# Kernel optimization log

Measured on AMD Instinct MI355X. Metric: run time of the kernel, lower is better.

Reference implementation:

```python
import jax, jax.numpy as jnp
import numpy as np

# 7 axial hex directions (dy, dx) including center, matching HexConv2d.DIRS
DIRS = [(0, 0), (1, 0), (0, 1), (-1, 1), (-1, 0), (0, -1), (1, -1)]


def _shift(x, dy, dx):
    """torch.roll-style shift with zero fill at wrapped edges. x: [B,C,H,W]."""
    sx, sy = -dx, -dy
    y = jnp.roll(x, shift=(sy, sx), axis=(2, 3))
    if sy > 0:
        y = y.at[:, :, :sy, :].set(0)
    elif sy < 0:
        y = y.at[:, :, sy:, :].set(0)
    if sx > 0:
        y = y.at[:, :, :, :sx].set(0)
    elif sx < 0:
        y = y.at[:, :, :, sx:].set(0)
    return y


def _hex_mask(H, dtype):
    size = H // 2
    q = jnp.arange(-size, size + 1)
    Q, R = jnp.meshgrid(q, q, indexing='ij')
    S = -Q - R
    # |Q|<=size and |R|<=size hold by construction; only |S|<=size cuts corners
    mask = ((jnp.abs(Q) <= size) & (jnp.abs(R) <= size) & (jnp.abs(S) <= size))
    return mask.astype(dtype)[None, None]  # [1,1,H,W]


def setup_inputs() -> dict:
    key = jax.random.key(0)
    k1, k2, k3 = jax.random.split(key, 3)
    B, Cin, Cout, H = 32, 256, 256, 49
    x = jax.random.normal(k1, (B, Cin, H, H), dtype=jnp.float32)
    weight = jax.random.normal(k2, (Cout, Cin, 7), dtype=jnp.float32) * 0.02
    bias = jax.random.normal(k3, (Cout,), dtype=jnp.float32) * 0.02
    return {"x": x, "weight": weight, "bias": bias}


def reference(x, weight, bias):
    mask = _hex_mask(x.shape[2], x.dtype)          # [1,1,H,W]
    x = x * mask
    # [7,B,C,H,W]: shifted+masked neighbor maps
    nbr = jnp.stack([_shift(x, dy, dx) for (dy, dx) in DIRS], axis=0) * mask
    # fused 1x1 conv over (channel, direction): weight [O,C,7]
    y = jnp.einsum('nbchw,ocn->bohw', nbr, weight) + bias[None, :, None, None]
    return y * mask
```

## Files before the change

### kernel.cpp

```cpp
#include <hip/hip_runtime.h>


typedef __attribute__((ext_vector_type(8))) short short8;
typedef __attribute__((ext_vector_type(4))) float floatx4;

#define NPIX   2401
#define PTILE  64
#define NPT    38
#define NSEG   11
#define WINROWS (NSEG*16)
#define ZROW   176
#define PADROWS 2560
#define PADBASE 64
#define XB_BYTES 41943040ULL
#define WS_NEED  (XB_BYTES + 917504ULL)

__device__ __forceinline__ unsigned short f2bf(float f) {
  unsigned u = __builtin_bit_cast(unsigned, f);
  u += 0x7fffu + ((u >> 16) & 1u);
  return (unsigned short)(u >> 16);
}

__device__ __forceinline__ bool hexmask(int gp) {
  int h = gp / 49;
  int w = gp - h * 49;
  int s = h + w;
  return (s >= 24 && s <= 72);
}

__global__ void prep_w_kernel(const float* __restrict__ w, unsigned short* __restrict__ wp) {
  int t = blockIdx.x * 256 + threadIdx.x;
  int l  = t & 63;
  int ot = (t >> 6) & 15;
  int kc = (t >> 10) & 7;
  int n  = t >> 13;
  int o  = ot * 16 + (l & 15);
  int cb = kc * 32 + ((l >> 4) * 8);
  const float* src = w + (size_t)(o * 256 + cb) * 7 + n;
  short8 pk;
#pragma unroll
  for (int j = 0; j < 8; ++j) pk[j] = (short)f2bf(src[j * 7]);
  ((short8*)wp)[t] = pk;
}

__global__ __launch_bounds__(256)
void prep_x_kernel(const float* __restrict__ x, unsigned short* __restrict__ xb) {
  __shared__ unsigned short t[64][72];
  const int b    = blockIdx.y;
  const int row0 = blockIdx.x * 64;
  const int gp0  = row0 - PADBASE;
  const int tid  = threadIdx.x;
  const int chl  = tid >> 2;
  const int pgrp = (tid & 3) * 16;
  const int pixw = tid >> 2;
  const int cgrp = (tid & 3) * 16;

  for (int ct = 0; ct < 4; ++ct) {
    int ch = ct * 64 + chl;
    const float* src = x + ((size_t)(b * 256 + ch)) * NPIX;
    unsigned short v[16];
#pragma unroll
    for (int j = 0; j < 16; ++j) {
      int gp = gp0 + pgrp + j;
      float f = (gp >= 0 && gp < NPIX && hexmask(gp)) ? src[gp] : 0.f;
      v[j] = f2bf(f);
    }
    __syncthreads();
#pragma unroll
    for (int j = 0; j < 16; ++j) t[chl][pgrp + j] = v[j];
    __syncthreads();
    short8 o0, o1;
#pragma unroll
    for (int j = 0; j < 8; ++j) o0[j] = (short)t[cgrp + j][pixw];
#pragma unroll
    for (int j = 0; j < 8; ++j) o1[j] = (short)t[cgrp + 8 + j][pixw];
    unsigned short* dst = xb + ((size_t)b * PADROWS + row0 + pixw) * 256 + ct * 64 + cgrp;
    *(short8*)dst = o0;
    *(short8*)(dst + 8) = o1;
  }
}

__global__ __launch_bounds__(256)
void hexconv_v2(const unsigned short* __restrict__ xb,
                const unsigned short* __restrict__ wp,
                const float* __restrict__ bias,
                float* __restrict__ out) {
  __shared__ __attribute__((aligned(16))) unsigned char smem[(ZROW + 1) * 64];

  const int tid  = threadIdx.x;
  const int lane = tid & 63;
  const int wv   = tid >> 6;
  const int col  = lane & 15;
  const int quad = lane >> 4;

  const int pt = blockIdx.x;
  const int b  = blockIdx.y;
  const int P0 = pt * PTILE;
  const int win_start = P0 - 52;

  if (tid < 16) ((unsigned*)smem)[ZROW * 16 + tid] = 0;

  const int OFF[7] = {0, 49, 1, -48, -49, -1, 48};
  const int DXP = (1 << 2) | (1 << 3);
  const int DXN = (1 << 5) | (1 << 6);

  int baddr[4][7];
#pragma unroll
  for (int j = 0; j < 4; ++j) {
    int pix = P0 + j * 16 + col;
    int wj = pix % 49;
    int rowbase = j * 16 + col + 52;
#pragma unroll
    for (int n = 0; n < 7; ++n) {
      bool bad = (((DXP >> n) & 1) && wj == 48) || (((DXN >> n) & 1) && wj == 0);
      int r = rowbase + OFF[n];
      int pp = (quad ^ ((r >> 1) & 3)) & 3;
      baddr[j][n] = bad ? (ZROW * 64 + quad * 16) : (r * 64 + pp * 16);
    }
  }

  const int gpart = (lane & 3) ^ ((lane >> 3) & 3);
  const unsigned short* xbrow = xb + ((size_t)b * PADROWS + PADBASE + win_start) * 256;
  const char* gsrc0 = (const char*)xbrow + (lane >> 2) * 512 + gpart * 16;

  floatx4 acc[4][4];
#pragma unroll
  for (int i = 0; i < 4; ++i)
#pragma unroll
    for (int j = 0; j < 4; ++j) acc[i][j] = (floatx4){0.f, 0.f, 0.f, 0.f};

  const char* wbase = (const char*)wp + ((size_t)(wv * 4) * 64 + lane) * 16;

  for (int kc = 0; kc < 8; ++kc) {
    __syncthreads();
#pragma unroll
    for (int s = wv; s < NSEG; s += 4) {
      const char* g = gsrc0 + (size_t)s * (16 * 512) + kc * 64;
      __builtin_amdgcn_global_load_lds(
          (const __attribute__((address_space(1))) unsigned int*)g,
          (__attribute__((address_space(3))) unsigned int*)(smem + s * 1024),
          16, 0, 0);
    }
    __syncthreads();
#pragma unroll
    for (int n = 0; n < 7; ++n) {
      short8 af[4];
#pragma unroll
      for (int i = 0; i < 4; ++i)
        af[i] = *(const short8*)(wbase + ((size_t)((n * 8 + kc) * 16 + i)) * 1024);
      short8 bf[4];
#pragma unroll
      for (int j = 0; j < 4; ++j)
        bf[j] = *(const short8*)(smem + baddr[j][n]);
#pragma unroll
      for (int i = 0; i < 4; ++i)
#pragma unroll
        for (int j = 0; j < 4; ++j)
          acc[i][j] = __builtin_amdgcn_mfma_f32_16x16x32_bf16(af[i], bf[j], acc[i][j], 0, 0, 0);
    }
  }

  const int ob = wv * 64;
  floatx4 bv[4];
#pragma unroll
  for (int i = 0; i < 4; ++i)
    bv[i] = *(const floatx4*)(bias + ob + i * 16 + quad * 4);

#pragma unroll
  for (int j = 0; j < 4; ++j) {
    int pix = P0 + j * 16 + col;
    if (pix >= NPIX) continue;
    int h = pix / 49;
    int w = pix - h * 49;
    bool m = (h + w >= 24 && h + w <= 72);
#pragma unroll
    for (int i = 0; i < 4; ++i) {
      int o = ob + i * 16 + quad * 4;
      float* dst = out + ((size_t)(b * 256 + o)) * NPIX + pix;
#pragma unroll
      for (int r = 0; r < 4; ++r) {
        float v = m ? (acc[i][j][r] + bv[i][r]) : 0.f;
        dst[(size_t)r * NPIX] = v;
      }
    }
  }
}

#define PITCH  40
#define V1WIN  168
#define V1ZROW 168
__global__ __launch_bounds__(256)
void hexconv_v1(const float* __restrict__ x,
                const unsigned short* __restrict__ wp,
                const float* __restrict__ bias,
                float* __restrict__ out) {
  __shared__ unsigned short sm[(V1ZROW + 2) * PITCH];
  const int tid = threadIdx.x, lane = tid & 63, wv = tid >> 6;
  const int col = lane & 15, quad = lane >> 4;
  const int pt = blockIdx.x, b = blockIdx.y;
  const int P0 = pt * PTILE, win_start = P0 - 52;
  if (tid < PITCH * 2) sm[V1ZROW * PITCH + tid] = 0;
  const int OFF[7] = {0, 49, 1, -48, -49, -1, 48};
  const int DXP = (1 << 2) | (1 << 3), DXN = (1 << 5) | (1 << 6);
  int baddr[4][7];
#pragma unroll
  for (int j = 0; j < 4; ++j) {
    int pix = P0 + j * 16 + col;
    int wj = pix % 49;
    int rowbase = pix - win_start;
#pragma unroll
    for (int n = 0; n < 7; ++n) {
      bool bad = (((DXP >> n) & 1) && wj == 48) || (((DXN >> n) & 1) && wj == 0);
      int row = bad ? V1ZROW : (rowbase + OFF[n]);
      baddr[j][n] = row * (PITCH * 2) + quad * 16;
    }
  }
  int sp[3], sgp[3]; bool sok[3];
#pragma unroll
  for (int pi = 0; pi < 3; ++pi) {
    int p = lane + pi * 64, gp = win_start + p;
    sp[pi] = p; sgp[pi] = gp;
    sok[pi] = (p < V1WIN) && (gp >= 0) && (gp < NPIX) && hexmask(gp);
  }
  floatx4 acc[4][4];
#pragma unroll
  for (int i = 0; i < 4; ++i)
#pragma unroll
    for (int j = 0; j < 4; ++j) acc[i][j] = (floatx4){0.f, 0.f, 0.f, 0.f};
  const short8* wpv = (const short8*)wp;
  const int wslot = wv * 4;
  for (int kc = 0; kc < 8; ++kc) {
    __syncthreads();
#pragma unroll
    for (int ci = 0; ci < 8; ++ci) {
      int c = ci * 4 + wv;
      const float* src = x + ((size_t)(b * 256 + kc * 32 + c)) * NPIX;
#pragma unroll
      for (int pi = 0; pi < 3; ++pi) {
        if (sp[pi] < V1WIN) {
          float v = sok[pi] ? src[sgp[pi]] : 0.f;
          sm[sp[pi] * PITCH + c] = f2bf(v);
        }
      }
    }
    __syncthreads();
#pragma unroll
    for (int n = 0; n < 7; ++n) {
      short8 af[4];
#pragma unroll
      for (int i = 0; i < 4; ++i)
        af[i] = wpv[((size_t)((n * 8 + kc) * 16 + wslot + i)) * 64 + lane];
      short8 bf[4];
#pragma unroll
      for (int j = 0; j < 4; ++j)
        bf[j] = *(const short8*)((const char*)sm + baddr[j][n]);
#pragma unroll
      for (int i = 0; i < 4; ++i)
#pragma unroll
        for (int j = 0; j < 4; ++j)
          acc[i][j] = __builtin_amdgcn_mfma_f32_16x16x32_bf16(af[i], bf[j], acc[i][j], 0, 0, 0);
    }
  }
  const int ob = wv * 64;
  floatx4 bv[4];
#pragma unroll
  for (int i = 0; i < 4; ++i)
    bv[i] = *(const floatx4*)(bias + ob + i * 16 + quad * 4);
#pragma unroll
  for (int j = 0; j < 4; ++j) {
    int pix = P0 + j * 16 + col;
    if (pix >= NPIX) continue;
    int h = pix / 49, w = pix - h * 49;
    bool m = (h + w >= 24 && h + w <= 72);
#pragma unroll
    for (int i = 0; i < 4; ++i) {
      int o = ob + i * 16 + quad * 4;
      float* dst = out + ((size_t)(b * 256 + o)) * NPIX + pix;
#pragma unroll
      for (int r = 0; r < 4; ++r) {
        float v = m ? (acc[i][j][r] + bv[i][r]) : 0.f;
        dst[(size_t)r * NPIX] = v;
      }
    }
  }
}

extern "C" void kernel_launch(void* const* d_in, const int* in_sizes, int n_in,
                              void* d_out, int out_size, void* d_ws, size_t ws_size,
                              hipStream_t stream) {
  const float* x    = (const float*)d_in[0];
  const float* w    = (const float*)d_in[1];
  const float* bias = (const float*)d_in[2];
  float* out = (float*)d_out;

  if (ws_size >= WS_NEED) {
    unsigned short* xb = (unsigned short*)d_ws;
    unsigned short* wp = (unsigned short*)((char*)d_ws + XB_BYTES);
    prep_x_kernel<<<dim3(PADROWS / 64, 32), 256, 0, stream>>>(x, xb);
    prep_w_kernel<<<224, 256, 0, stream>>>(w, wp);
    hexconv_v2<<<dim3(NPT, 32), 256, 0, stream>>>(xb, wp, bias, out);
  } else {
    unsigned short* wp = (unsigned short*)d_ws;
    prep_w_kernel<<<224, 256, 0, stream>>>(w, wp);
    hexconv_v1<<<dim3(NPT, 32), 256, 0, stream>>>(x, wp, bias, out);
  }
}
```

Baseline: 286.7 us.

## Pad rows to width 50, double-buffer LDS, and widen pixel tile to 128

Lays out the bf16 activation buffer with one zero pad column per row (stride 50). Neighbour shifts then need no per-pixel edge checks and every lane uses one base address per direction. The main kernel doubles its pixel tile to 128 and double-buffers the LDS staging so the next channel chunk loads during compute. It also prefetches weight fragments one step ahead and staggers the starting chunk per block. This raises register use (32 accumulators per lane) and adds a separate pad-zeroing kernel, and the grid drops to 20x32 blocks, which may underfill the GPU.

```diff
diff --git a/kernel.cpp b/kernel.cpp
--- a/kernel.cpp
+++ b/kernel.cpp
@@ -2,30 +2,26 @@
 
 
 typedef __attribute__((ext_vector_type(8))) short short8;
+typedef __attribute__((ext_vector_type(4))) short short4v;
 typedef __attribute__((ext_vector_type(4))) float floatx4;
 
 #define NPIX   2401
-#define PTILE  64
-#define NPT    38
-#define NSEG   11
-#define WINROWS (NSEG*16)
-#define ZROW   176
-#define PADROWS 2560
-#define PADBASE 64
-#define XB_BYTES 41943040ULL
-#define WS_NEED  (XB_BYTES + 917504ULL)
+#define W50    50
+#define PREAL  2450
+#define XBLEAD 56
+#define XBROWS 2672
+#define PT3    128
+#define NT3    20
+#define NSEG3  15
+#define BUFB   (NSEG3*1024)
+#define XB3_BYTES ((size_t)32*XBROWS*256*2)
+#define WP_BYTES  917504ULL
+#define WS_NEED3  (XB3_BYTES + WP_BYTES)
 
 __device__ __forceinline__ unsigned short f2bf(float f) {
   unsigned u = __builtin_bit_cast(unsigned, f);
   u += 0x7fffu + ((u >> 16) & 1u);
   return (unsigned short)(u >> 16);
-}
-
-__device__ __forceinline__ bool hexmask(int gp) {
-  int h = gp / 49;
-  int w = gp - h * 49;
-  int s = h + w;
-  return (s >= 24 && s <= 72);
 }
 
 __global__ void prep_w_kernel(const float* __restrict__ w, unsigned short* __restrict__ wp) {
@@ -43,49 +39,77 @@
   ((short8*)wp)[t] = pk;
 }
 
+__global__ void zero_pads(unsigned short* __restrict__ xb) {
+  int idx = blockIdx.x * 256 + threadIdx.x;
+  int c16 = idx & 31;
+  int rb  = idx >> 5;
+  int row = rb % XBROWS;
+  int b   = rb / XBROWS;
+  int p   = row - XBLEAD;
+  bool pad = (p < 0) || (p >= PREAL) || (p % W50 == 49);
+  if (pad) {
+    short8 z = {0,0,0,0,0,0,0,0};
+    *(short8*)(xb + ((size_t)b * XBROWS + row) * 256 + c16 * 8) = z;
+  }
+}
+
 __global__ __launch_bounds__(256)
-void prep_x_kernel(const float* __restrict__ x, unsigned short* __restrict__ xb) {
-  __shared__ unsigned short t[64][72];
-  const int b    = blockIdx.y;
-  const int row0 = blockIdx.x * 64;
-  const int gp0  = row0 - PADBASE;
-  const int tid  = threadIdx.x;
-  const int chl  = tid >> 2;
-  const int pgrp = (tid & 3) * 16;
-  const int pixw = tid >> 2;
-  const int cgrp = (tid & 3) * 16;
-
-  for (int ct = 0; ct < 4; ++ct) {
-    int ch = ct * 64 + chl;
-    const float* src = x + ((size_t)(b * 256 + ch)) * NPIX;
-    unsigned short v[16];
-#pragma unroll
-    for (int j = 0; j < 16; ++j) {
-      int gp = gp0 + pgrp + j;
-      float f = (gp >= 0 && gp < NPIX && hexmask(gp)) ? src[gp] : 0.f;
-      v[j] = f2bf(f);
-    }
-    __syncthreads();
-#pragma unroll
-    for (int j = 0; j < 16; ++j) t[chl][pgrp + j] = v[j];
-    __syncthreads();
+void prep_x3(const float* __restrict__ x, unsigned short* __restrict__ xb) {
+  __shared__ unsigned short t[64][68];
+  const int tid = threadIdx.x;
+  const int span = blockIdx.x, cg = blockIdx.y, b = blockIdx.z;
+  const int s0 = span * 64;
+  {
+    const int chl = tid >> 2, i4 = tid & 3;
+    const float* src = x + ((size_t)(b * 256 + cg * 64 + chl)) * NPIX;
+#pragma unroll
+    for (int it = 0; it < 4; ++it) {
+      int pxl = it * 16 + i4 * 4;
+      int r = s0 + pxl;
+      float vv[4] = {0.f, 0.f, 0.f, 0.f};
+      if (r + 3 < NPIX) {
+        float4 v = *(const float4*)(src + r);
+        vv[0] = v.x; vv[1] = v.y; vv[2] = v.z; vv[3] = v.w;
+      } else {
+#pragma unroll
+        for (int e = 0; e < 4; ++e) if (r + e < NPIX) vv[e] = src[r + e];
+      }
+      short4v u = {0, 0, 0, 0};
+#pragma unroll
+      for (int e = 0; e < 4; ++e) {
+        int re = r + e;
+        unsigned short uu = 0;
+        if (re < NPIX) {
+          int h = re / 49, w = re - h * 49, s = h + w;
+          if (s >= 24 && s <= 72) uu = f2bf(vv[e]);
+        }
+        u[e] = (short)uu;
+      }
+      *(short4v*)&t[chl][pxl] = u;
+    }
+  }
+  __syncthreads();
+  const int rl = tid >> 2, cpart = tid & 3;
+  const int r = s0 + rl;
+  if (r < NPIX) {
+    int p = r + r / 49;
+    unsigned short* dst = xb + ((size_t)b * XBROWS + (p + XBLEAD)) * 256 + cg * 64 + cpart * 16;
     short8 o0, o1;
 #pragma unroll
-    for (int j = 0; j < 8; ++j) o0[j] = (short)t[cgrp + j][pixw];
-#pragma unroll
-    for (int j = 0; j < 8; ++j) o1[j] = (short)t[cgrp + 8 + j][pixw];
-    unsigned short* dst = xb + ((size_t)b * PADROWS + row0 + pixw) * 256 + ct * 64 + cgrp;
+    for (int k = 0; k < 8; ++k) o0[k] = (short)t[cpart * 16 + k][rl];
+#pragma unroll
+    for (int k = 0; k < 8; ++k) o1[k] = (short)t[cpart * 16 + 8 + k][rl];
     *(short8*)dst = o0;
     *(short8*)(dst + 8) = o1;
   }
 }
 
-__global__ __launch_bounds__(256)
-void hexconv_v2(const unsigned short* __restrict__ xb,
+__global__ __launch_bounds__(256, 2)
+void hexconv_v3(const unsigned short* __restrict__ xb,
                 const unsigned short* __restrict__ wp,
                 const float* __restrict__ bias,
                 float* __restrict__ out) {
-  __shared__ __attribute__((aligned(16))) unsigned char smem[(ZROW + 1) * 64];
+  __shared__ __attribute__((aligned(16))) unsigned char smem[2 * BUFB];
 
   const int tid  = threadIdx.x;
   const int lane = tid & 63;
@@ -95,92 +119,94 @@
 
   const int pt = blockIdx.x;
   const int b  = blockIdx.y;
-  const int P0 = pt * PTILE;
-  const int win_start = P0 - 52;
-
-  if (tid < 16) ((unsigned*)smem)[ZROW * 16 + tid] = 0;
-
-  const int OFF[7] = {0, 49, 1, -48, -49, -1, 48};
-  const int DXP = (1 << 2) | (1 << 3);
-  const int DXN = (1 << 5) | (1 << 6);
-
-  int baddr[4][7];
-#pragma unroll
-  for (int j = 0; j < 4; ++j) {
-    int pix = P0 + j * 16 + col;
-    int wj = pix % 49;
-    int rowbase = j * 16 + col + 52;
+  const int P0 = pt * PT3;
+  const int phase = (pt + b * 3) & 7;
+
+  const int OFF[7] = {0, 50, 1, -49, -50, -1, 49};
+
+  int ba[7];
+#pragma unroll
+  for (int n = 0; n < 7; ++n) {
+    int r0 = col + 56 + OFF[n];
+    int r64 = r0 << 6;
+    ba[n] = (r64 + quad * 16) ^ ((r64 >> 3) & 0x30);
+  }
+
+  const int gpart = (lane & 3) ^ ((lane >> 3) & 3);
+  const char* gsrc0 = (const char*)(xb + ((size_t)b * XBROWS + (size_t)P0) * 256)
+                      + (lane >> 2) * 512 + gpart * 16;
+
+  auto stage = [&](int buf, int kc) {
+    char* ldsb = (char*)smem + buf * BUFB;
+    for (int s = wv; s < NSEG3; s += 4)
+      __builtin_amdgcn_global_load_lds(
+          (const __attribute__((address_space(1))) unsigned int*)(gsrc0 + (size_t)s * 8192 + kc * 64),
+          (__attribute__((address_space(3))) unsigned int*)(ldsb + s * 1024), 16, 0, 0);
+  };
+
+  const char* wbase = (const char*)wp + (size_t)(wv * 4) * 1024 + lane * 16;
+  auto loadA = [&](int kc, int n, short8* dst) {
+#pragma unroll
+    for (int ii = 0; ii < 4; ++ii)
+      dst[ii] = *(const short8*)(wbase + ((size_t)((n * 8 + kc) * 16 + ii)) * 1024);
+  };
+
+  floatx4 acc[4][8];
+#pragma unroll
+  for (int ii = 0; ii < 4; ++ii)
+#pragma unroll
+    for (int j = 0; j < 8; ++j) acc[ii][j] = (floatx4){0.f, 0.f, 0.f, 0.f};
+
+  stage(0, phase);
+  short8 afc[4];
+  loadA(phase, 0, afc);
+  __syncthreads();
+
+  for (int i = 0; i < 8; ++i) {
+    const int kc  = (i + phase) & 7;
+    const int kcn = (i + 1 + phase) & 7;
+    if (i < 7) stage((i + 1) & 1, kcn);
+    const char* bufp = (const char*)smem + (i & 1) * BUFB;
 #pragma unroll
     for (int n = 0; n < 7; ++n) {
-      bool bad = (((DXP >> n) & 1) && wj == 48) || (((DXN >> n) & 1) && wj == 0);
-      int r = rowbase + OFF[n];
-      int pp = (quad ^ ((r >> 1) & 3)) & 3;
-      baddr[j][n] = bad ? (ZROW * 64 + quad * 16) : (r * 64 + pp * 16);
-    }
-  }
-
-  const int gpart = (lane & 3) ^ ((lane >> 3) & 3);
-  const unsigned short* xbrow = xb + ((size_t)b * PADROWS + PADBASE + win_start) * 256;
-  const char* gsrc0 = (const char*)xbrow + (lane >> 2) * 512 + gpart * 16;
-
-  floatx4 acc[4][4];
-#pragma unroll
-  for (int i = 0; i < 4; ++i)
-#pragma unroll
-    for (int j = 0; j < 4; ++j) acc[i][j] = (floatx4){0.f, 0.f, 0.f, 0.f};
-
-  const char* wbase = (const char*)wp + ((size_t)(wv * 4) * 64 + lane) * 16;
-
-  for (int kc = 0; kc < 8; ++kc) {
+      short8 afn[4];
+      loadA((n < 6) ? kc : kcn, (n < 6) ? n + 1 : 0, afn);
+      short8 bf[8];
+#pragma unroll
+      for (int j = 0; j < 8; ++j)
+        bf[j] = *(const short8*)(bufp + ba[n] + j * 1024);
+#pragma unroll
+      for (int ii = 0; ii < 4; ++ii)
+#pragma unroll
+        for (int j = 0; j < 8; ++j)
+          acc[ii][j] = __builtin_amdgcn_mfma_f32_16x16x32_bf16(afc[ii], bf[j], acc[ii][j], 0, 0, 0);
+#pragma unroll
+      for (int ii = 0; ii < 4; ++ii) afc[ii] = afn[ii];
+    }
     __syncthreads();
-#pragma unroll
-    for (int s = wv; s < NSEG; s += 4) {
-      const char* g = gsrc0 + (size_t)s * (16 * 512) + kc * 64;
-      __builtin_amdgcn_global_load_lds(
-          (const __attribute__((address_space(1))) unsigned int*)g,
-          (__attribute__((address_space(3))) unsigned int*)(smem + s * 1024),
-          16, 0, 0);
-    }
-    __syncthreads();
-#pragma unroll
-    for (int n = 0; n < 7; ++n) {
-      short8 af[4];
-#pragma unroll
-      for (int i = 0; i < 4; ++i)
-        af[i] = *(const short8*)(wbase + ((size_t)((n * 8 + kc) * 16 + i)) * 1024);
-      short8 bf[4];
-#pragma unroll
-      for (int j = 0; j < 4; ++j)
-        bf[j] = *(const short8*)(smem + baddr[j][n]);
-#pragma unroll
-      for (int i = 0; i < 4; ++i)
-#pragma unroll
-        for (int j = 0; j < 4; ++j)
-          acc[i][j] = __builtin_amdgcn_mfma_f32_16x16x32_bf16(af[i], bf[j], acc[i][j], 0, 0, 0);
-    }
   }
 
   const int ob = wv * 64;
   floatx4 bv[4];
 #pragma unroll
-  for (int i = 0; i < 4; ++i)
-    bv[i] = *(const floatx4*)(bias + ob + i * 16 + quad * 4);
-
-#pragma unroll
-  for (int j = 0; j < 4; ++j) {
-    int pix = P0 + j * 16 + col;
-    if (pix >= NPIX) continue;
-    int h = pix / 49;
-    int w = pix - h * 49;
-    bool m = (h + w >= 24 && h + w <= 72);
-#pragma unroll
-    for (int i = 0; i < 4; ++i) {
-      int o = ob + i * 16 + quad * 4;
-      float* dst = out + ((size_t)(b * 256 + o)) * NPIX + pix;
-#pragma unroll
-      for (int r = 0; r < 4; ++r) {
-        float v = m ? (acc[i][j][r] + bv[i][r]) : 0.f;
-        dst[(size_t)r * NPIX] = v;
+  for (int ii = 0; ii < 4; ++ii)
+    bv[ii] = *(const floatx4*)(bias + ob + ii * 16 + quad * 4);
+
+#pragma unroll
+  for (int j = 0; j < 8; ++j) {
+    int p = P0 + j * 16 + col;
+    int h = p / W50;
+    int w = p - h * W50;
+    if (w >= 49 || p >= PREAL) continue;
+    bool m = (h + w >= 24) && (h + w <= 72);
+    size_t ridx = (size_t)h * 49 + w;
+#pragma unroll
+    for (int ii = 0; ii < 4; ++ii) {
+      float* dst = out + ((size_t)(b * 256 + ob + ii * 16 + quad * 4)) * NPIX + ridx;
+#pragma unroll
+      for (int rr = 0; rr < 4; ++rr) {
+        float v = m ? (acc[ii][j][rr] + bv[ii][rr]) : 0.f;
+        dst[(size_t)rr * NPIX] = v;
       }
     }
   }
@@ -198,7 +224,7 @@
   const int tid = threadIdx.x, lane = tid & 63, wv = tid >> 6;
   const int col = lane & 15, quad = lane >> 4;
   const int pt = blockIdx.x, b = blockIdx.y;
-  const int P0 = pt * PTILE, win_start = P0 - 52;
+  const int P0 = pt * 64, win_start = P0 - 52;
   if (tid < PITCH * 2) sm[V1ZROW * PITCH + tid] = 0;
   const int OFF[7] = {0, 49, 1, -48, -49, -1, 48};
   const int DXP = (1 << 2) | (1 << 3), DXN = (1 << 5) | (1 << 6);
@@ -220,7 +246,9 @@
   for (int pi = 0; pi < 3; ++pi) {
     int p = lane + pi * 64, gp = win_start + p;
     sp[pi] = p; sgp[pi] = gp;
-    sok[pi] = (p < V1WIN) && (gp >= 0) && (gp < NPIX) && hexmask(gp);
+    bool hm = false;
+    if (gp >= 0 && gp < NPIX) { int h = gp / 49, w = gp - h * 49, s = h + w; hm = (s >= 24 && s <= 72); }
+    sok[pi] = (p < V1WIN) && hm;
   }
   floatx4 acc[4][4];
 #pragma unroll
@@ -293,15 +321,16 @@
   const float* bias = (const float*)d_in[2];
   float* out = (float*)d_out;
 
-  if (ws_size >= WS_NEED) {
+  if (ws_size >= WS_NEED3) {
     unsigned short* xb = (unsigned short*)d_ws;
-    unsigned short* wp = (unsigned short*)((char*)d_ws + XB_BYTES);
-    prep_x_kernel<<<dim3(PADROWS / 64, 32), 256, 0, stream>>>(x, xb);
+    unsigned short* wp = (unsigned short*)((char*)d_ws + XB3_BYTES);
+    zero_pads<<<(32 * XBROWS * 32) / 256, 256, 0, stream>>>(xb);
     prep_w_kernel<<<224, 256, 0, stream>>>(w, wp);
-    hexconv_v2<<<dim3(NPT, 32), 256, 0, stream>>>(xb, wp, bias, out);
+    prep_x3<<<dim3(38, 4, 32), 256, 0, stream>>>(x, xb);
+    hexconv_v3<<<dim3(NT3, 32), 256, 0, stream>>>(xb, wp, bias, out);
   } else {
     unsigned short* wp = (unsigned short*)d_ws;
     prep_w_kernel<<<224, 256, 0, stream>>>(w, wp);
-    hexconv_v1<<<dim3(NPT, 32), 256, 0, stream>>>(x, wp, bias, out);
-  }
-}
+    hexconv_v1<<<dim3(38, 32), 256, 0, stream>>>(x, wp, bias, out);
+  }
+}
```

Result: faster. 239.0 us (-16.6%).
